# Kernel tuning notes

Hardware: AMD Instinct MI355X
Metric: run time of the kernel (lower is better)

Reference implementation:

```python
import jax, jax.numpy as jnp
import numpy as np

WIN = 9  # win_size from init

def setup_inputs() -> dict:
    key = jax.random.key(0)
    ks = jax.random.split(key, 4)
    N, L, C, U = 8, 4096, 256, 256
    x = jax.random.normal(ks[0], (N, L, C), dtype=jnp.float32)
    W_qry = jax.random.normal(ks[1], (C, U), dtype=jnp.float32) * 0.05
    W_key = jax.random.normal(ks[2], (C, U), dtype=jnp.float32) * 0.05
    v = jax.random.normal(ks[3], (U,), dtype=jnp.float32) * 0.05
    b = jnp.zeros((U,), dtype=jnp.float32)
    return {"x": x, "W_qry": W_qry, "W_key": W_key, "v": v, "b": b}

def reference(x, W_qry, W_key, v, b):
    N, L, C = x.shape
    n_w = L - WIN + 1
    # sliding-window gather: idx[w, s] = w + s
    idx = jnp.arange(n_w)[:, None] + jnp.arange(WIN)[None, :]
    x_win = x[:, idx]
    x_ctr = x[:, WIN // 2 : WIN // 2 + n_w]                    # [N, n_w, C]
    key = jnp.einsum('nwsc,cu->nwsu', x_win, W_key)
    qry = jnp.einsum('nwc,cu->nwu', x_ctr, W_qry)              # [N, n_w, U]
    score = jnp.einsum('nwsu,u->nws', jnp.tanh(qry[:, :, None, :] + key + b), v)
    weight = jax.nn.softmax(score, axis=2)                     # softmax over window dim
    out = jnp.einsum('nwsc,nws->nwc', x_win, weight)           # [N, n_w, C]
    return out
```

## Files before the change

kernel.cpp:

```cpp
#include <hip/hip_runtime.h>
#include <hip/hip_bf16.h>

#define WIN   9
#define NB    8
#define LL    4096
#define CC    256
#define UU    256
#define NW    (LL - WIN + 1)
#define MROWS (NB * LL)

#define BM 128
#define BK 64

typedef unsigned short ushort;
typedef __attribute__((ext_vector_type(8))) unsigned short ushort8v;
typedef __attribute__((ext_vector_type(4))) unsigned short ushort4v;
typedef __attribute__((ext_vector_type(8))) short short8v;
typedef __attribute__((ext_vector_type(4))) float f32x4;

__device__ __forceinline__ float bf16_to_f(ushort u) {
    return __uint_as_float(((unsigned int)u) << 16);
}
__device__ __forceinline__ ushort f2bf(float f) {
    __hip_bfloat16 h = __float2bfloat16(f);
    return *reinterpret_cast<ushort*>(&h);
}
__device__ __forceinline__ float fast_tanh(float x) {
    float e = __expf(2.0f * x);
    return 1.0f - 2.0f * __builtin_amdgcn_rcpf(e + 1.0f);
}

__global__ __launch_bounds__(256) void cvt_x(const float* __restrict__ X,
                                             ushort* __restrict__ Xb) {
    size_t i = ((size_t)blockIdx.x * 256 + threadIdx.x) * 8;
    float4 v0 = *reinterpret_cast<const float4*>(X + i);
    float4 v1 = *reinterpret_cast<const float4*>(X + i + 4);
    ushort8v o;
    o[0] = f2bf(v0.x); o[1] = f2bf(v0.y); o[2] = f2bf(v0.z); o[3] = f2bf(v0.w);
    o[4] = f2bf(v1.x); o[5] = f2bf(v1.y); o[6] = f2bf(v1.z); o[7] = f2bf(v1.w);
    *reinterpret_cast<ushort8v*>(Xb + i) = o;
}

__global__ __launch_bounds__(256) void transpose_w(const float* __restrict__ Wk,
                                                   const float* __restrict__ Wq,
                                                   ushort* __restrict__ WkT,
                                                   ushort* __restrict__ WqT) {
    const float* W = blockIdx.z ? Wq : Wk;
    ushort* O = blockIdx.z ? WqT : WkT;
    __shared__ float t[32][33];
    int c0 = blockIdx.x * 32, u0 = blockIdx.y * 32;
    int tr = threadIdx.x >> 3, tc = (threadIdx.x & 7) * 4;
    float4 v = *reinterpret_cast<const float4*>(&W[(size_t)(c0 + tr) * UU + u0 + tc]);
    t[tr][tc + 0] = v.x; t[tr][tc + 1] = v.y; t[tr][tc + 2] = v.z; t[tr][tc + 3] = v.w;
    __syncthreads();
    ushort4v o;
    #pragma unroll
    for (int i = 0; i < 4; ++i) o[i] = f2bf(t[tc + i][tr]);
    *reinterpret_cast<ushort4v*>(&O[(size_t)(u0 + tr) * CC + c0 + tc]) = o;
}

__global__ __launch_bounds__(256, 2) void gemm_lds(const ushort* __restrict__ Xb,
                                                   const ushort* __restrict__ WTall,
                                                   ushort* __restrict__ Kout,
                                                   ushort* __restrict__ Qout) {
    const int m0 = (blockIdx.x & 255) * BM;
    const int nt = blockIdx.x >> 8;
    const int n0 = nt * 128;

    __shared__ ushort As[BM * BK];
    __shared__ ushort Bs[BM * BK];

    const int tid = threadIdx.x;
    const int wid = tid >> 6, lane = tid & 63;
    const int wr = wid >> 1, wc = wid & 1;
    const int lrow = lane & 15;
    const int lkc  = lane >> 4;

    const int srow_in_issue = wid * 8 + (lane >> 3);
    const int schunk = lane & 7;

    f32x4 acc[4][4] = {};

    for (int k0 = 0; k0 < CC; k0 += BK) {
        #pragma unroll
        for (int i = 0; i < 4; ++i) {
            int row = i * 32 + srow_in_issue;
            int ca  = schunk ^ (row & 7);
            const ushort* srcA = Xb    + (size_t)(m0 + row) * CC + k0 + ca * 8;
            const ushort* srcB = WTall + (size_t)(n0 + row) * CC + k0 + ca * 8;
            ushort* dstA = As + i * 2048 + wid * 512;
            ushort* dstB = Bs + i * 2048 + wid * 512;
            __builtin_amdgcn_global_load_lds(
                (const __attribute__((address_space(1))) void*)srcA,
                (__attribute__((address_space(3))) void*)dstA, 16, 0, 0);
            __builtin_amdgcn_global_load_lds(
                (const __attribute__((address_space(1))) void*)srcB,
                (__attribute__((address_space(3))) void*)dstB, 16, 0, 0);
        }
        __syncthreads();

        #pragma unroll
        for (int ks = 0; ks < 2; ++ks) {
            short8v af[4], bq[4];
            #pragma unroll
            for (int m = 0; m < 4; ++m) {
                int r = wr * 64 + m * 16 + lrow;
                int cc = ks * 4 + lkc;
                af[m] = *reinterpret_cast<const short8v*>(As + r * 64 + (cc ^ (r & 7)) * 8);
            }
            #pragma unroll
            for (int n = 0; n < 4; ++n) {
                int r = wc * 64 + n * 16 + lrow;
                int cc = ks * 4 + lkc;
                bq[n] = *reinterpret_cast<const short8v*>(Bs + r * 64 + (cc ^ (r & 7)) * 8);
            }
            #pragma unroll
            for (int m = 0; m < 4; ++m)
                #pragma unroll
                for (int n = 0; n < 4; ++n)
                    acc[m][n] = __builtin_amdgcn_mfma_f32_16x16x32_bf16(af[m], bq[n], acc[m][n], 0, 0, 0);
        }
        __syncthreads();
    }

    ushort* Out = (nt < 2) ? Kout : Qout;
    const int colbase = (nt & 1) * 128 + wc * 64;
    const int rowbase = m0 + wr * 64 + (lane >> 4) * 4;
    #pragma unroll
    for (int m = 0; m < 4; ++m)
        #pragma unroll
        for (int n = 0; n < 4; ++n)
            #pragma unroll
            for (int j = 0; j < 4; ++j)
                Out[(size_t)(rowbase + m * 16 + j) * UU + colbase + n * 16 + lrow] =
                    f2bf(acc[m][n][j]);
}

__global__ __launch_bounds__(256) void attn_smooth(
    const ushort* __restrict__ Xb,
    const ushort* __restrict__ Kb,
    const ushort* __restrict__ Qb,
    const float* __restrict__ v,
    const float* __restrict__ b,
    float* __restrict__ out) {
    const int wave = threadIdx.x >> 6;
    const int lane = threadIdx.x & 63;
    const int bid = blockIdx.x;
    const int nb = (bid & 7) * 1022 + (bid >> 3);
    const int item = nb * 4 + wave;
    const int n = item / NW;
    const int w = item % NW;
    const int u0 = lane * 4;

    const size_t rowbase = (size_t)(n * LL + w);

    float4 bv = *reinterpret_cast<const float4*>(&b[u0]);
    float4 vv = *reinterpret_cast<const float4*>(&v[u0]);

    ushort4 qu = *reinterpret_cast<const ushort4*>(&Qb[(rowbase + WIN / 2) * UU + u0]);
    float qb0 = bf16_to_f(qu.x) + bv.x;
    float qb1 = bf16_to_f(qu.y) + bv.y;
    float qb2 = bf16_to_f(qu.z) + bv.z;
    float qb3 = bf16_to_f(qu.w) + bv.w;

    float p[WIN];
    #pragma unroll
    for (int s = 0; s < WIN; ++s) {
        ushort4 ku = *reinterpret_cast<const ushort4*>(&Kb[(rowbase + s) * UU + u0]);
        float t;
        t  = vv.x * fast_tanh(qb0 + bf16_to_f(ku.x));
        t += vv.y * fast_tanh(qb1 + bf16_to_f(ku.y));
        t += vv.z * fast_tanh(qb2 + bf16_to_f(ku.z));
        t += vv.w * fast_tanh(qb3 + bf16_to_f(ku.w));
        p[s] = t;
    }
    #pragma unroll
    for (int off = 32; off; off >>= 1)
        #pragma unroll
        for (int s = 0; s < WIN; ++s)
            p[s] += __shfl_xor(p[s], off);

    float m = p[0];
    #pragma unroll
    for (int s = 1; s < WIN; ++s) m = fmaxf(m, p[s]);
    float e[WIN];
    float sum = 0.0f;
    #pragma unroll
    for (int s = 0; s < WIN; ++s) { e[s] = __expf(p[s] - m); sum += e[s]; }
    float inv = 1.0f / sum;

    float4 acc = {0.0f, 0.0f, 0.0f, 0.0f};
    #pragma unroll
    for (int s = 0; s < WIN; ++s) {
        float ws = e[s] * inv;
        ushort4 xv = *reinterpret_cast<const ushort4*>(&Xb[(rowbase + s) * CC + u0]);
        acc.x = fmaf(ws, bf16_to_f(xv.x), acc.x);
        acc.y = fmaf(ws, bf16_to_f(xv.y), acc.y);
        acc.z = fmaf(ws, bf16_to_f(xv.z), acc.z);
        acc.w = fmaf(ws, bf16_to_f(xv.w), acc.w);
    }
    *reinterpret_cast<float4*>(&out[((size_t)n * NW + w) * CC + u0]) = acc;
}

extern "C" void kernel_launch(void* const* d_in, const int* in_sizes, int n_in,
                              void* d_out, int out_size, void* d_ws, size_t ws_size,
                              hipStream_t stream) {
    const float* x  = (const float*)d_in[0];
    const float* Wq = (const float*)d_in[1];
    const float* Wk = (const float*)d_in[2];
    const float* v  = (const float*)d_in[3];
    const float* b  = (const float*)d_in[4];
    float* out = (float*)d_out;

    const size_t MU = (size_t)MROWS * UU;
    ushort* Kbuf = (ushort*)d_ws;
    ushort* Qbuf = Kbuf + MU;
    ushort* Xb   = Qbuf + MU;
    ushort* WkT  = Xb + MU;
    ushort* WqT  = WkT + (size_t)CC * UU;

    cvt_x<<<MROWS * CC / (256 * 8), 256, 0, stream>>>(x, Xb);
    transpose_w<<<dim3(8, 8, 2), 256, 0, stream>>>(Wk, Wq, WkT, WqT);
    gemm_lds<<<1024, 256, 0, stream>>>(Xb, WkT, Kbuf, Qbuf);
    attn_smooth<<<(NB * NW) / 4, 256, 0, stream>>>(Xb, Kbuf, Qbuf, v, b, out);
}
```

Measured before the change: 145.7 us.

## Double-buffer GEMM LDS tiles and pack four windows per wave in attention

The projection GEMM now uses two LDS buffers so global-to-LDS loads of the next K tile are issued before computing on the current one, with one fewer barrier per iteration. The attention kernel assigns 16 lanes per window with 16 channels each, so a wave handles four windows, loads use 16-byte vectors, and the cross-lane reduction shrinks to four shuffle steps. Block-to-XCD mapping is reworked for the new grid. This costs doubled LDS for the GEMM and more registers per thread in attention, which could lower occupancy.

```diff
diff --git a/kernel.cpp b/kernel.cpp
--- a/kernel.cpp
+++ b/kernel.cpp
@@ -67,8 +67,8 @@
     const int nt = blockIdx.x >> 8;
     const int n0 = nt * 128;
 
-    __shared__ ushort As[BM * BK];
-    __shared__ ushort Bs[BM * BK];
+    __shared__ ushort As[2][BM * BK];
+    __shared__ ushort Bs[2][BM * BK];
 
     const int tid = threadIdx.x;
     const int wid = tid >> 6, lane = tid & 63;
@@ -76,20 +76,20 @@
     const int lrow = lane & 15;
     const int lkc  = lane >> 4;
 
-    const int srow_in_issue = wid * 8 + (lane >> 3);
+    const int srow = wid * 8 + (lane >> 3);
     const int schunk = lane & 7;
 
     f32x4 acc[4][4] = {};
 
-    for (int k0 = 0; k0 < CC; k0 += BK) {
+    auto stage = [&](int bi, int k0) {
         #pragma unroll
         for (int i = 0; i < 4; ++i) {
-            int row = i * 32 + srow_in_issue;
+            int row = i * 32 + srow;
             int ca  = schunk ^ (row & 7);
             const ushort* srcA = Xb    + (size_t)(m0 + row) * CC + k0 + ca * 8;
             const ushort* srcB = WTall + (size_t)(n0 + row) * CC + k0 + ca * 8;
-            ushort* dstA = As + i * 2048 + wid * 512;
-            ushort* dstB = Bs + i * 2048 + wid * 512;
+            ushort* dstA = &As[bi][i * 2048 + wid * 512];
+            ushort* dstB = &Bs[bi][i * 2048 + wid * 512];
             __builtin_amdgcn_global_load_lds(
                 (const __attribute__((address_space(1))) void*)srcA,
                 (__attribute__((address_space(3))) void*)dstA, 16, 0, 0);
@@ -97,7 +97,15 @@
                 (const __attribute__((address_space(1))) void*)srcB,
                 (__attribute__((address_space(3))) void*)dstB, 16, 0, 0);
         }
-        __syncthreads();
+    };
+
+    stage(0, 0);
+    __syncthreads();
+
+    #pragma unroll
+    for (int t = 0; t < 4; ++t) {
+        const int cur = t & 1;
+        if (t < 3) stage(cur ^ 1, (t + 1) * BK);
 
         #pragma unroll
         for (int ks = 0; ks < 2; ++ks) {
@@ -106,13 +114,13 @@
             for (int m = 0; m < 4; ++m) {
                 int r = wr * 64 + m * 16 + lrow;
                 int cc = ks * 4 + lkc;
-                af[m] = *reinterpret_cast<const short8v*>(As + r * 64 + (cc ^ (r & 7)) * 8);
+                af[m] = *reinterpret_cast<const short8v*>(&As[cur][r * 64 + (cc ^ (r & 7)) * 8]);
             }
             #pragma unroll
             for (int n = 0; n < 4; ++n) {
                 int r = wc * 64 + n * 16 + lrow;
                 int cc = ks * 4 + lkc;
-                bq[n] = *reinterpret_cast<const short8v*>(Bs + r * 64 + (cc ^ (r & 7)) * 8);
+                bq[n] = *reinterpret_cast<const short8v*>(&Bs[cur][r * 64 + (cc ^ (r & 7)) * 8]);
             }
             #pragma unroll
             for (int m = 0; m < 4; ++m)
@@ -120,7 +128,7 @@
                 for (int n = 0; n < 4; ++n)
                     acc[m][n] = __builtin_amdgcn_mfma_f32_16x16x32_bf16(af[m], bq[n], acc[m][n], 0, 0, 0);
         }
-        __syncthreads();
+        if (t < 3) __syncthreads();
     }
 
     ushort* Out = (nt < 2) ? Kout : Qout;
@@ -145,37 +153,53 @@
     float* __restrict__ out) {
     const int wave = threadIdx.x >> 6;
     const int lane = threadIdx.x & 63;
+    const int g = lane >> 4;
+    const int t = lane & 15;
     const int bid = blockIdx.x;
-    const int nb = (bid & 7) * 1022 + (bid >> 3);
-    const int item = nb * 4 + wave;
+    const int xcd = bid & 7, o8 = bid >> 3;
+    const int nb = (xcd < 4 ? xcd * 256 : 1024 + (xcd - 4) * 255) + o8;
+    const int item = nb * 16 + wave * 4 + g;
     const int n = item / NW;
-    const int w = item % NW;
-    const int u0 = lane * 4;
-
-    const size_t rowbase = (size_t)(n * LL + w);
-
-    float4 bv = *reinterpret_cast<const float4*>(&b[u0]);
-    float4 vv = *reinterpret_cast<const float4*>(&v[u0]);
-
-    ushort4 qu = *reinterpret_cast<const ushort4*>(&Qb[(rowbase + WIN / 2) * UU + u0]);
-    float qb0 = bf16_to_f(qu.x) + bv.x;
-    float qb1 = bf16_to_f(qu.y) + bv.y;
-    float qb2 = bf16_to_f(qu.z) + bv.z;
-    float qb3 = bf16_to_f(qu.w) + bv.w;
+    const int w = item - n * NW;
+    const int u0 = t * 16;
+
+    const size_t rowbase = (size_t)n * LL + w;
+
+    float bb[16], vv[16];
+    #pragma unroll
+    for (int i = 0; i < 4; ++i) {
+        *reinterpret_cast<float4*>(&bb[i * 4]) = *reinterpret_cast<const float4*>(b + u0 + i * 4);
+        *reinterpret_cast<float4*>(&vv[i * 4]) = *reinterpret_cast<const float4*>(v + u0 + i * 4);
+    }
+
+    float qb[16];
+    {
+        const ushort* qrow = Qb + (rowbase + WIN / 2) * UU + u0;
+        ushort8v q0 = *reinterpret_cast<const ushort8v*>(qrow);
+        ushort8v q1 = *reinterpret_cast<const ushort8v*>(qrow + 8);
+        #pragma unroll
+        for (int i = 0; i < 8; ++i) {
+            qb[i]     = bf16_to_f(q0[i]) + bb[i];
+            qb[8 + i] = bf16_to_f(q1[i]) + bb[8 + i];
+        }
+    }
 
     float p[WIN];
     #pragma unroll
     for (int s = 0; s < WIN; ++s) {
-        ushort4 ku = *reinterpret_cast<const ushort4*>(&Kb[(rowbase + s) * UU + u0]);
-        float t;
-        t  = vv.x * fast_tanh(qb0 + bf16_to_f(ku.x));
-        t += vv.y * fast_tanh(qb1 + bf16_to_f(ku.y));
-        t += vv.z * fast_tanh(qb2 + bf16_to_f(ku.z));
-        t += vv.w * fast_tanh(qb3 + bf16_to_f(ku.w));
-        p[s] = t;
-    }
-    #pragma unroll
-    for (int off = 32; off; off >>= 1)
+        const ushort* krow = Kb + (rowbase + s) * UU + u0;
+        ushort8v k0 = *reinterpret_cast<const ushort8v*>(krow);
+        ushort8v k1 = *reinterpret_cast<const ushort8v*>(krow + 8);
+        float a = 0.0f;
+        #pragma unroll
+        for (int i = 0; i < 8; ++i) {
+            a += vv[i]     * fast_tanh(qb[i]     + bf16_to_f(k0[i]));
+            a += vv[8 + i] * fast_tanh(qb[8 + i] + bf16_to_f(k1[i]));
+        }
+        p[s] = a;
+    }
+    #pragma unroll
+    for (int off = 8; off; off >>= 1)
         #pragma unroll
         for (int s = 0; s < WIN; ++s)
             p[s] += __shfl_xor(p[s], off);
@@ -189,17 +213,23 @@
     for (int s = 0; s < WIN; ++s) { e[s] = __expf(p[s] - m); sum += e[s]; }
     float inv = 1.0f / sum;
 
-    float4 acc = {0.0f, 0.0f, 0.0f, 0.0f};
+    float acc[16] = {};
     #pragma unroll
     for (int s = 0; s < WIN; ++s) {
         float ws = e[s] * inv;
-        ushort4 xv = *reinterpret_cast<const ushort4*>(&Xb[(rowbase + s) * CC + u0]);
-        acc.x = fmaf(ws, bf16_to_f(xv.x), acc.x);
-        acc.y = fmaf(ws, bf16_to_f(xv.y), acc.y);
-        acc.z = fmaf(ws, bf16_to_f(xv.z), acc.z);
-        acc.w = fmaf(ws, bf16_to_f(xv.w), acc.w);
-    }
-    *reinterpret_cast<float4*>(&out[((size_t)n * NW + w) * CC + u0]) = acc;
+        const ushort* xrow = Xb + (rowbase + s) * CC + u0;
+        ushort8v x0 = *reinterpret_cast<const ushort8v*>(xrow);
+        ushort8v x1 = *reinterpret_cast<const ushort8v*>(xrow + 8);
+        #pragma unroll
+        for (int i = 0; i < 8; ++i) {
+            acc[i]     = fmaf(ws, bf16_to_f(x0[i]), acc[i]);
+            acc[8 + i] = fmaf(ws, bf16_to_f(x1[i]), acc[8 + i]);
+        }
+    }
+    float* orow = out + ((size_t)n * NW + w) * CC + u0;
+    #pragma unroll
+    for (int i = 0; i < 4; ++i)
+        *reinterpret_cast<float4*>(orow + i * 4) = *reinterpret_cast<const float4*>(&acc[i * 4]);
 }
 
 extern "C" void kernel_launch(void* const* d_in, const int* in_sizes, int n_in,
@@ -222,5 +252,5 @@
     cvt_x<<<MROWS * CC / (256 * 8), 256, 0, stream>>>(x, Xb);
     transpose_w<<<dim3(8, 8, 2), 256, 0, stream>>>(Wk, Wq, WkT, WqT);
     gemm_lds<<<1024, 256, 0, stream>>>(Xb, WkT, Kbuf, Qbuf);
-    attn_smooth<<<(NB * NW) / 4, 256, 0, stream>>>(Xb, Kbuf, Qbuf, v, b, out);
-}
+    attn_smooth<<<2044, 256, 0, stream>>>(Xb, Kbuf, Qbuf, v, b, out);
+}
```

Result: faster. 136.0 us (-6.7%).
